# Performance work log

Hardware: AMD Instinct MI355X
Metric: run time of the kernel (lower is better)

The kernel has to match this reference:

```python
import jax, jax.numpy as jnp
import numpy as np


def make_base_grid(D, H, W, dtype):
    # torch.affine_grid(align_corners=True) base coords: last dim is (x, y, z)
    # where x varies along W, y along H, z along D, each in [-1, 1].
    zs = jnp.linspace(-1.0, 1.0, D, dtype=dtype)
    ys = jnp.linspace(-1.0, 1.0, H, dtype=dtype)
    xs = jnp.linspace(-1.0, 1.0, W, dtype=dtype)
    gz, gy, gx = jnp.meshgrid(zs, ys, xs, indexing='ij')  # each (D,H,W)
    return jnp.stack([gx, gy, gz], axis=-1)  # (D,H,W,3)


def trilinear_sample(vol, grid):
    # vol: (C,D,H,W); grid: (D,H,W,3) normalized coords (x,y,z);
    # align_corners=True, padding_mode='zeros' (torch grid_sample defaults).
    C, D, H, W = vol.shape
    ix = (grid[..., 0] + 1.0) * 0.5 * (W - 1)
    iy = (grid[..., 1] + 1.0) * 0.5 * (H - 1)
    iz = (grid[..., 2] + 1.0) * 0.5 * (D - 1)
    ix0f, iy0f, iz0f = jnp.floor(ix), jnp.floor(iy), jnp.floor(iz)
    wx, wy, wz = ix - ix0f, iy - iy0f, iz - iz0f
    ix0, iy0, iz0 = ix0f.astype(jnp.int32), iy0f.astype(jnp.int32), iz0f.astype(jnp.int32)
    ix1, iy1, iz1 = ix0 + 1, iy0 + 1, iz0 + 1

    def corner(zi, yi, xi, w):
        valid = ((zi >= 0) & (zi < D) & (yi >= 0) & (yi < H) & (xi >= 0) & (xi < W))
        zc = jnp.clip(zi, 0, D - 1)
        yc = jnp.clip(yi, 0, H - 1)
        xc = jnp.clip(xi, 0, W - 1)
        v = vol[:, zc, yc, xc]  # (C,D,H,W)
        return v * (w * valid.astype(vol.dtype))[None]

    one = jnp.asarray(1.0, vol.dtype)
    out = (corner(iz0, iy0, ix0, (one - wz) * (one - wy) * (one - wx))
           + corner(iz0, iy0, ix1, (one - wz) * (one - wy) * wx)
           + corner(iz0, iy1, ix0, (one - wz) * wy * (one - wx))
           + corner(iz0, iy1, ix1, (one - wz) * wy * wx)
           + corner(iz1, iy0, ix0, wz * (one - wy) * (one - wx))
           + corner(iz1, iy0, ix1, wz * (one - wy) * wx)
           + corner(iz1, iy1, ix0, wz * wy * (one - wx))
           + corner(iz1, iy1, ix1, wz * wy * wx))
    return out  # (C,D,H,W)


def setup_inputs() -> dict:
    key = jax.random.key(0)
    kx, ky = jax.random.split(key)
    shape = (1, 1, 192, 192, 192)
    x = jax.random.uniform(kx, shape, dtype=jnp.float32)
    y = jax.random.uniform(ky, shape, dtype=jnp.float32)
    return {"x": x, "y": y}


def reference(x, y):
    N, C, D, H, W = x.shape
    base = make_base_grid(D, H, W, x.dtype)  # (D,H,W,3) == identity affine_grid
    xv = x[:, 0]  # (N,D,H,W), channel 0 only as in the torch code
    yv = y[:, 0]
    x_sum = jnp.sum(x)
    y_sum = jnp.sum(y)
    # weighted center of mass for each normalized coordinate (x,y,z)
    cm_x = jnp.einsum('ndhw,dhwk->k', xv, base) / x_sum  # (3,)
    cm_y = jnp.einsum('ndhw,dhwk->k', yv, base) / y_sum  # (3,)
    t = cm_x - cm_y  # translation placed in theta[:, :, 3]
    grid = base + t  # (D,H,W,3): affine_grid with identity + translation
    grid_b = jnp.broadcast_to(grid[None], (N, D, H, W, 3))
    transformed = jax.vmap(trilinear_sample)(x, grid_b)  # (N,C,D,H,W)
    return transformed, grid_b
```

## Files before the change

### kernel.cpp

```cpp
#include <hip/hip_runtime.h>
#include <math.h>

#define DD 192
#define HH 192
#define WW 192
#define NVOX (DD*HH*WW)
#define NV4  (NVOX/4)
#define RB   1024
#define RT   256

struct Consts {
    float tx, ty, tz;
    float wgt[8];
    int   dx0, dy0, dz0;
};

__device__ __forceinline__ float gcoord(int i, int n) {
    return -1.0f + (float)i * (2.0f / (float)(n - 1));
}

__global__ void reduce_kernel(const float* __restrict__ x,
                              const float* __restrict__ y,
                              double* __restrict__ partials) {
    double acc[8] = {0,0,0,0,0,0,0,0};
    int tid = blockIdx.x * blockDim.x + threadIdx.x;
    const float4* x4 = (const float4*)x;
    const float4* y4 = (const float4*)y;
    for (int i = tid; i < NV4; i += RB * RT) {
        float4 xv = x4[i];
        float4 yv = y4[i];
        int base = i * 4;
        int w = base % WW;
        int rem = base / WW;
        int h = rem % HH;
        int d = rem / HH;
        float gy = gcoord(h, HH);
        float gz = gcoord(d, DD);
        float xs[4] = {xv.x, xv.y, xv.z, xv.w};
        float ys[4] = {yv.x, yv.y, yv.z, yv.w};
        #pragma unroll
        for (int k = 0; k < 4; ++k) {
            float gx = gcoord(w + k, WW);
            acc[0] += (double)xs[k];
            acc[1] += (double)(xs[k] * gx);
            acc[2] += (double)(xs[k] * gy);
            acc[3] += (double)(xs[k] * gz);
            acc[4] += (double)ys[k];
            acc[5] += (double)(ys[k] * gx);
            acc[6] += (double)(ys[k] * gy);
            acc[7] += (double)(ys[k] * gz);
        }
    }
    #pragma unroll
    for (int q = 0; q < 8; ++q) {
        double v = acc[q];
        #pragma unroll
        for (int off = 32; off > 0; off >>= 1)
            v += __shfl_down(v, off, 64);
        acc[q] = v;
    }
    __shared__ double lds[4][8];
    int lane = threadIdx.x & 63;
    int wave = threadIdx.x >> 6;
    if (lane == 0) {
        #pragma unroll
        for (int q = 0; q < 8; ++q) lds[wave][q] = acc[q];
    }
    __syncthreads();
    if (threadIdx.x < 8) {
        int q = threadIdx.x;
        partials[q * RB + blockIdx.x] = lds[0][q] + lds[1][q] + lds[2][q] + lds[3][q];
    }
}

__global__ void finalize_kernel(const double* __restrict__ partials,
                                Consts* __restrict__ cs) {
    double s[8];
    #pragma unroll
    for (int q = 0; q < 8; ++q) {
        double v = 0.0;
        for (int i = threadIdx.x; i < RB; i += 256) v += partials[q * RB + i];
        #pragma unroll
        for (int off = 32; off > 0; off >>= 1)
            v += __shfl_down(v, off, 64);
        s[q] = v;
    }
    __shared__ double lds[4][8];
    int lane = threadIdx.x & 63;
    int wave = threadIdx.x >> 6;
    if (lane == 0) {
        #pragma unroll
        for (int q = 0; q < 8; ++q) lds[wave][q] = s[q];
    }
    __syncthreads();
    if (threadIdx.x == 0) {
        double sums[8];
        #pragma unroll
        for (int q = 0; q < 8; ++q)
            sums[q] = lds[0][q] + lds[1][q] + lds[2][q] + lds[3][q];
        double tx = sums[1] / sums[0] - sums[5] / sums[4];
        double ty = sums[2] / sums[0] - sums[6] / sums[4];
        double tz = sums[3] / sums[0] - sums[7] / sums[4];
        cs->tx = (float)tx; cs->ty = (float)ty; cs->tz = (float)tz;
        double cx = tx * (double)(WW - 1) * 0.5;
        double cy = ty * (double)(HH - 1) * 0.5;
        double cz = tz * (double)(DD - 1) * 0.5;
        double fx = floor(cx), fy = floor(cy), fz = floor(cz);
        float wx = (float)(cx - fx), wy = (float)(cy - fy), wz = (float)(cz - fz);
        cs->dx0 = (int)fx; cs->dy0 = (int)fy; cs->dz0 = (int)fz;
        #pragma unroll
        for (int k = 0; k < 8; ++k) {
            float wzz = (k & 4) ? wz : 1.0f - wz;
            float wyy = (k & 2) ? wy : 1.0f - wy;
            float wxx = (k & 1) ? wx : 1.0f - wx;
            cs->wgt[k] = wzz * wyy * wxx;
        }
    }
}

__global__ void __launch_bounds__(256) main_kernel(const float* __restrict__ x,
                                                   const Consts* __restrict__ csp,
                                                   float* __restrict__ out_t,
                                                   float4* __restrict__ out_g4) {
    __shared__ float gbuf[768];
    const Consts c = *csp;
    int idx = blockIdx.x * 256 + threadIdx.x;
    int w = idx % WW;
    int rem = idx / WW;
    int h = rem % HH;
    int d = rem / HH;
    float gx = gcoord(w, WW) + c.tx;
    float gy = gcoord(h, HH) + c.ty;
    float gz = gcoord(d, DD) + c.tz;
    gbuf[3 * threadIdx.x + 0] = gx;
    gbuf[3 * threadIdx.x + 1] = gy;
    gbuf[3 * threadIdx.x + 2] = gz;
    __syncthreads();
    if (threadIdx.x < 192) {
        const float4* src = (const float4*)gbuf;
        out_g4[blockIdx.x * 192 + threadIdx.x] = src[threadIdx.x];
    }
    int xi0 = w + c.dx0, yi0 = h + c.dy0, zi0 = d + c.dz0;
    int xi1 = xi0 + 1,  yi1 = yi0 + 1,  zi1 = zi0 + 1;
    int xs0 = min(max(xi0, 0), WW - 1), xs1 = min(max(xi1, 0), WW - 1);
    int ys0 = min(max(yi0, 0), HH - 1), ys1 = min(max(yi1, 0), HH - 1);
    int zs0 = min(max(zi0, 0), DD - 1), zs1 = min(max(zi1, 0), DD - 1);
    float vx0 = ((unsigned)xi0 < (unsigned)WW) ? 1.0f : 0.0f;
    float vx1 = ((unsigned)xi1 < (unsigned)WW) ? 1.0f : 0.0f;
    float vy0 = ((unsigned)yi0 < (unsigned)HH) ? 1.0f : 0.0f;
    float vy1 = ((unsigned)yi1 < (unsigned)HH) ? 1.0f : 0.0f;
    float vz0 = ((unsigned)zi0 < (unsigned)DD) ? 1.0f : 0.0f;
    float vz1 = ((unsigned)zi1 < (unsigned)DD) ? 1.0f : 0.0f;
    int rb00 = (zs0 * HH + ys0) * WW;
    int rb01 = (zs0 * HH + ys1) * WW;
    int rb10 = (zs1 * HH + ys0) * WW;
    int rb11 = (zs1 * HH + ys1) * WW;
    float acc =
        x[rb00 + xs0] * (c.wgt[0] * (vz0 * vy0 * vx0)) +
        x[rb00 + xs1] * (c.wgt[1] * (vz0 * vy0 * vx1)) +
        x[rb01 + xs0] * (c.wgt[2] * (vz0 * vy1 * vx0)) +
        x[rb01 + xs1] * (c.wgt[3] * (vz0 * vy1 * vx1)) +
        x[rb10 + xs0] * (c.wgt[4] * (vz1 * vy0 * vx0)) +
        x[rb10 + xs1] * (c.wgt[5] * (vz1 * vy0 * vx1)) +
        x[rb11 + xs0] * (c.wgt[6] * (vz1 * vy1 * vx0)) +
        x[rb11 + xs1] * (c.wgt[7] * (vz1 * vy1 * vx1));
    out_t[idx] = acc;
}

extern "C" void kernel_launch(void* const* d_in, const int* in_sizes, int n_in,
                              void* d_out, int out_size, void* d_ws, size_t ws_size,
                              hipStream_t stream) {
    const float* x = (const float*)d_in[0];
    const float* y = (const float*)d_in[1];
    float* out = (float*)d_out;
    float* out_t = out;
    float4* out_g4 = (float4*)(out + NVOX);
    double* partials = (double*)d_ws;
    Consts* cs = (Consts*)((char*)d_ws + 8 * RB * sizeof(double));
    reduce_kernel<<<RB, RT, 0, stream>>>(x, y, partials);
    finalize_kernel<<<1, 256, 0, stream>>>(partials, cs);
    main_kernel<<<NVOX / 256, 256, 0, stream>>>(x, cs, out_t, out_g4);
}
```

Before: 176.1 us.

## Fuse finalize into reduce via atomics; compute four outputs per thread in sampler

Drops the separate finalize kernel. Each reduce block now atomically adds its partial sums to a global buffer, and the last block (found with an atomic counter) computes the translation constants, at the cost of an extra memset. The reduce loop sums each float4 in fp32 before converting to double, which cuts double-precision adds. The sampler now handles four consecutive x-voxels per thread. It reuses five loaded neighbours per row, writes the grid directly as three float4s without LDS staging, and uses a nontemporal vector store for the output.

```diff
diff --git a/kernel.cpp b/kernel.cpp
--- a/kernel.cpp
+++ b/kernel.cpp
@@ -8,6 +8,8 @@
 #define NV4  (NVOX/4)
 #define RB   1024
 #define RT   256
+
+typedef float f4 __attribute__((ext_vector_type(4)));
 
 struct Consts {
     float tx, ty, tz;
@@ -21,7 +23,9 @@
 
 __global__ void reduce_kernel(const float* __restrict__ x,
                               const float* __restrict__ y,
-                              double* __restrict__ partials) {
+                              double* __restrict__ gsum,
+                              unsigned int* __restrict__ counter,
+                              Consts* __restrict__ cs) {
     double acc[8] = {0,0,0,0,0,0,0,0};
     int tid = blockIdx.x * blockDim.x + threadIdx.x;
     const float4* x4 = (const float4*)x;
@@ -38,18 +42,21 @@
         float gz = gcoord(d, DD);
         float xs[4] = {xv.x, xv.y, xv.z, xv.w};
         float ys[4] = {yv.x, yv.y, yv.z, yv.w};
+        float sx = 0.f, sy = 0.f, sxg = 0.f, syg = 0.f;
         #pragma unroll
         for (int k = 0; k < 4; ++k) {
             float gx = gcoord(w + k, WW);
-            acc[0] += (double)xs[k];
-            acc[1] += (double)(xs[k] * gx);
-            acc[2] += (double)(xs[k] * gy);
-            acc[3] += (double)(xs[k] * gz);
-            acc[4] += (double)ys[k];
-            acc[5] += (double)(ys[k] * gx);
-            acc[6] += (double)(ys[k] * gy);
-            acc[7] += (double)(ys[k] * gz);
+            sx += xs[k]; sxg = fmaf(xs[k], gx, sxg);
+            sy += ys[k]; syg = fmaf(ys[k], gx, syg);
         }
+        acc[0] += (double)sx;
+        acc[1] += (double)sxg;
+        acc[2] += (double)(sx * gy);
+        acc[3] += (double)(sx * gz);
+        acc[4] += (double)sy;
+        acc[5] += (double)syg;
+        acc[6] += (double)(sy * gy);
+        acc[7] += (double)(sy * gz);
     }
     #pragma unroll
     for (int q = 0; q < 8; ++q) {
@@ -69,102 +76,105 @@
     __syncthreads();
     if (threadIdx.x < 8) {
         int q = threadIdx.x;
-        partials[q * RB + blockIdx.x] = lds[0][q] + lds[1][q] + lds[2][q] + lds[3][q];
+        atomicAdd(&gsum[q], lds[0][q] + lds[1][q] + lds[2][q] + lds[3][q]);
     }
-}
-
-__global__ void finalize_kernel(const double* __restrict__ partials,
-                                Consts* __restrict__ cs) {
-    double s[8];
-    #pragma unroll
-    for (int q = 0; q < 8; ++q) {
-        double v = 0.0;
-        for (int i = threadIdx.x; i < RB; i += 256) v += partials[q * RB + i];
-        #pragma unroll
-        for (int off = 32; off > 0; off >>= 1)
-            v += __shfl_down(v, off, 64);
-        s[q] = v;
-    }
-    __shared__ double lds[4][8];
-    int lane = threadIdx.x & 63;
-    int wave = threadIdx.x >> 6;
-    if (lane == 0) {
-        #pragma unroll
-        for (int q = 0; q < 8; ++q) lds[wave][q] = s[q];
-    }
-    __syncthreads();
+    __threadfence();
     if (threadIdx.x == 0) {
-        double sums[8];
-        #pragma unroll
-        for (int q = 0; q < 8; ++q)
-            sums[q] = lds[0][q] + lds[1][q] + lds[2][q] + lds[3][q];
-        double tx = sums[1] / sums[0] - sums[5] / sums[4];
-        double ty = sums[2] / sums[0] - sums[6] / sums[4];
-        double tz = sums[3] / sums[0] - sums[7] / sums[4];
-        cs->tx = (float)tx; cs->ty = (float)ty; cs->tz = (float)tz;
-        double cx = tx * (double)(WW - 1) * 0.5;
-        double cy = ty * (double)(HH - 1) * 0.5;
-        double cz = tz * (double)(DD - 1) * 0.5;
-        double fx = floor(cx), fy = floor(cy), fz = floor(cz);
-        float wx = (float)(cx - fx), wy = (float)(cy - fy), wz = (float)(cz - fz);
-        cs->dx0 = (int)fx; cs->dy0 = (int)fy; cs->dz0 = (int)fz;
-        #pragma unroll
-        for (int k = 0; k < 8; ++k) {
-            float wzz = (k & 4) ? wz : 1.0f - wz;
-            float wyy = (k & 2) ? wy : 1.0f - wy;
-            float wxx = (k & 1) ? wx : 1.0f - wx;
-            cs->wgt[k] = wzz * wyy * wxx;
+        unsigned int old = atomicAdd(counter, 1u);
+        if (old == RB - 1) {
+            __threadfence();
+            double s[8];
+            #pragma unroll
+            for (int q = 0; q < 8; ++q)
+                s[q] = atomicAdd(&gsum[q], 0.0);
+            double tx = s[1]/s[0] - s[5]/s[4];
+            double ty = s[2]/s[0] - s[6]/s[4];
+            double tz = s[3]/s[0] - s[7]/s[4];
+            cs->tx = (float)tx; cs->ty = (float)ty; cs->tz = (float)tz;
+            double cx = tx * (double)(WW - 1) * 0.5;
+            double cy = ty * (double)(HH - 1) * 0.5;
+            double cz = tz * (double)(DD - 1) * 0.5;
+            double fx = floor(cx), fy = floor(cy), fz = floor(cz);
+            float wx = (float)(cx - fx), wy = (float)(cy - fy), wz = (float)(cz - fz);
+            cs->dx0 = (int)fx; cs->dy0 = (int)fy; cs->dz0 = (int)fz;
+            #pragma unroll
+            for (int k = 0; k < 8; ++k) {
+                float wzz = (k & 4) ? wz : 1.0f - wz;
+                float wyy = (k & 2) ? wy : 1.0f - wy;
+                float wxx = (k & 1) ? wx : 1.0f - wx;
+                cs->wgt[k] = wzz * wyy * wxx;
+            }
         }
     }
 }
 
 __global__ void __launch_bounds__(256) main_kernel(const float* __restrict__ x,
                                                    const Consts* __restrict__ csp,
-                                                   float* __restrict__ out_t,
-                                                   float4* __restrict__ out_g4) {
-    __shared__ float gbuf[768];
+                                                   f4* __restrict__ out_t4,
+                                                   f4* __restrict__ out_g4) {
     const Consts c = *csp;
     int idx = blockIdx.x * 256 + threadIdx.x;
-    int w = idx % WW;
-    int rem = idx / WW;
+    int wq  = idx % (WW / 4);
+    int rem = idx / (WW / 4);
     int h = rem % HH;
     int d = rem / HH;
-    float gx = gcoord(w, WW) + c.tx;
-    float gy = gcoord(h, HH) + c.ty;
-    float gz = gcoord(d, DD) + c.tz;
-    gbuf[3 * threadIdx.x + 0] = gx;
-    gbuf[3 * threadIdx.x + 1] = gy;
-    gbuf[3 * threadIdx.x + 2] = gz;
-    __syncthreads();
-    if (threadIdx.x < 192) {
-        const float4* src = (const float4*)gbuf;
-        out_g4[blockIdx.x * 192 + threadIdx.x] = src[threadIdx.x];
-    }
-    int xi0 = w + c.dx0, yi0 = h + c.dy0, zi0 = d + c.dz0;
-    int xi1 = xi0 + 1,  yi1 = yi0 + 1,  zi1 = zi0 + 1;
-    int xs0 = min(max(xi0, 0), WW - 1), xs1 = min(max(xi1, 0), WW - 1);
+    int w = wq * 4;
+
+    float gy  = gcoord(h, HH) + c.ty;
+    float gz  = gcoord(d, DD) + c.tz;
+    float gx0 = gcoord(w + 0, WW) + c.tx;
+    float gx1 = gcoord(w + 1, WW) + c.tx;
+    float gx2 = gcoord(w + 2, WW) + c.tx;
+    float gx3 = gcoord(w + 3, WW) + c.tx;
+    int gi = idx * 3;
+    out_g4[gi + 0] = (f4){gx0, gy, gz, gx1};
+    out_g4[gi + 1] = (f4){gy, gz, gx2, gy};
+    out_g4[gi + 2] = (f4){gz, gx3, gy, gz};
+
+    int zi0 = d + c.dz0, zi1 = zi0 + 1;
+    int yi0 = h + c.dy0, yi1 = yi0 + 1;
+    int zs0 = min(max(zi0, 0), DD - 1), zs1 = min(max(zi1, 0), DD - 1);
     int ys0 = min(max(yi0, 0), HH - 1), ys1 = min(max(yi1, 0), HH - 1);
-    int zs0 = min(max(zi0, 0), DD - 1), zs1 = min(max(zi1, 0), DD - 1);
-    float vx0 = ((unsigned)xi0 < (unsigned)WW) ? 1.0f : 0.0f;
-    float vx1 = ((unsigned)xi1 < (unsigned)WW) ? 1.0f : 0.0f;
-    float vy0 = ((unsigned)yi0 < (unsigned)HH) ? 1.0f : 0.0f;
-    float vy1 = ((unsigned)yi1 < (unsigned)HH) ? 1.0f : 0.0f;
-    float vz0 = ((unsigned)zi0 < (unsigned)DD) ? 1.0f : 0.0f;
-    float vz1 = ((unsigned)zi1 < (unsigned)DD) ? 1.0f : 0.0f;
+    float vz0 = ((unsigned)zi0 < (unsigned)DD) ? 1.f : 0.f;
+    float vz1 = ((unsigned)zi1 < (unsigned)DD) ? 1.f : 0.f;
+    float vy0 = ((unsigned)yi0 < (unsigned)HH) ? 1.f : 0.f;
+    float vy1 = ((unsigned)yi1 < (unsigned)HH) ? 1.f : 0.f;
+    float m00 = vz0 * vy0, m01 = vz0 * vy1, m10 = vz1 * vy0, m11 = vz1 * vy1;
+    float w0 = c.wgt[0] * m00, w1 = c.wgt[1] * m00;
+    float w2 = c.wgt[2] * m01, w3 = c.wgt[3] * m01;
+    float w4 = c.wgt[4] * m10, w5 = c.wgt[5] * m10;
+    float w6 = c.wgt[6] * m11, w7 = c.wgt[7] * m11;
     int rb00 = (zs0 * HH + ys0) * WW;
     int rb01 = (zs0 * HH + ys1) * WW;
     int rb10 = (zs1 * HH + ys0) * WW;
     int rb11 = (zs1 * HH + ys1) * WW;
-    float acc =
-        x[rb00 + xs0] * (c.wgt[0] * (vz0 * vy0 * vx0)) +
-        x[rb00 + xs1] * (c.wgt[1] * (vz0 * vy0 * vx1)) +
-        x[rb01 + xs0] * (c.wgt[2] * (vz0 * vy1 * vx0)) +
-        x[rb01 + xs1] * (c.wgt[3] * (vz0 * vy1 * vx1)) +
-        x[rb10 + xs0] * (c.wgt[4] * (vz1 * vy0 * vx0)) +
-        x[rb10 + xs1] * (c.wgt[5] * (vz1 * vy0 * vx1)) +
-        x[rb11 + xs0] * (c.wgt[6] * (vz1 * vy1 * vx0)) +
-        x[rb11 + xs1] * (c.wgt[7] * (vz1 * vy1 * vx1));
-    out_t[idx] = acc;
+
+    int s = w + c.dx0;
+    float r00[5], r01[5], r10[5], r11[5];
+    #pragma unroll
+    for (int j = 0; j < 5; ++j) {
+        int t = s + j;
+        int xc = min(max(t, 0), WW - 1);
+        float vx = ((unsigned)t < (unsigned)WW) ? 1.f : 0.f;
+        r00[j] = x[rb00 + xc] * vx;
+        r01[j] = x[rb01 + xc] * vx;
+        r10[j] = x[rb10 + xc] * vx;
+        r11[j] = x[rb11 + xc] * vx;
+    }
+    f4 o;
+    #pragma unroll
+    for (int k = 0; k < 4; ++k) {
+        float v = r00[k] * w0;
+        v = fmaf(r00[k + 1], w1, v);
+        v = fmaf(r01[k],     w2, v);
+        v = fmaf(r01[k + 1], w3, v);
+        v = fmaf(r10[k],     w4, v);
+        v = fmaf(r10[k + 1], w5, v);
+        v = fmaf(r11[k],     w6, v);
+        v = fmaf(r11[k + 1], w7, v);
+        o[k] = v;
+    }
+    __builtin_nontemporal_store(o, out_t4 + idx);
 }
 
 extern "C" void kernel_launch(void* const* d_in, const int* in_sizes, int n_in,
@@ -173,11 +183,12 @@
     const float* x = (const float*)d_in[0];
     const float* y = (const float*)d_in[1];
     float* out = (float*)d_out;
-    float* out_t = out;
-    float4* out_g4 = (float4*)(out + NVOX);
-    double* partials = (double*)d_ws;
-    Consts* cs = (Consts*)((char*)d_ws + 8 * RB * sizeof(double));
-    reduce_kernel<<<RB, RT, 0, stream>>>(x, y, partials);
-    finalize_kernel<<<1, 256, 0, stream>>>(partials, cs);
-    main_kernel<<<NVOX / 256, 256, 0, stream>>>(x, cs, out_t, out_g4);
+    f4* out_t4 = (f4*)out;
+    f4* out_g4 = (f4*)(out + NVOX);
+    double* gsum = (double*)d_ws;
+    unsigned int* counter = (unsigned int*)((char*)d_ws + 64);
+    Consts* cs = (Consts*)((char*)d_ws + 128);
+    hipMemsetAsync(d_ws, 0, 128, stream);
+    reduce_kernel<<<RB, RT, 0, stream>>>(x, y, gsum, counter, cs);
+    main_kernel<<<NV4 / 256, 256, 0, stream>>>(x, cs, out_t4, out_g4);
 }
```

Result: slower. 245.9 us (+39.7%).
